# Performance work log

Hardware: AMD Instinct MI355X
Metric: run time of the kernel (lower is better)

The kernel has to match this reference:

```python
import jax, jax.numpy as jnp
import numpy as np

N = 50000
E = 1_600_000
IN_C = 128
HID = 128
HEADS = 4
F_OUT = HID // HEADS  # 32
NEG_SLOPE = 0.2


def _glorot(key, shape):
    fan_in, fan_out = shape[0], shape[-1]
    lim = jnp.sqrt(6.0 / (fan_in + fan_out)).astype(jnp.float32)
    return jax.random.uniform(key, shape, jnp.float32, -lim, lim)


def setup_inputs() -> dict:
    key = jax.random.key(0)
    ks = jax.random.split(key, 12)
    x = jax.random.normal(ks[0], (N, IN_C), jnp.float32)
    edge_index = jax.random.randint(ks[1], (2, E), 0, N, jnp.int32)
    # layer 0 params
    W0 = _glorot(ks[2], (IN_C, HEADS * F_OUT))
    att_src0 = _glorot(ks[3], (HEADS, F_OUT))
    att_dst0 = _glorot(ks[4], (HEADS, F_OUT))
    b0 = jnp.zeros((HEADS * F_OUT,), jnp.float32)
    # layer 1 params
    W1 = _glorot(ks[5], (HID, HEADS * F_OUT))
    att_src1 = _glorot(ks[6], (HEADS, F_OUT))
    att_dst1 = _glorot(ks[7], (HEADS, F_OUT))
    b1 = jnp.zeros((HEADS * F_OUT,), jnp.float32)
    return {"x": x, "edge_index": edge_index,
            "W0": W0, "att_src0": att_src0, "att_dst0": att_dst0, "b0": b0,
            "W1": W1, "att_src1": att_src1, "att_dst1": att_dst1, "b1": b1}


def gat_conv(x, src, dst, W, att_src, att_dst, b):
    n = x.shape[0]
    h = (x @ W).reshape(n, HEADS, F_OUT)              # [N,H,F]
    a_s = jnp.einsum('nhf,hf->nh', h, att_src)        # [N,H]
    a_d = jnp.einsum('nhf,hf->nh', h, att_dst)        # [N,H]
    e = jax.nn.leaky_relu(a_s[src] + a_d[dst], NEG_SLOPE)   # [E,H]
    # segment softmax over destination-node neighborhoods
    e_max = jax.ops.segment_max(e, dst, num_segments=n)     # [N,H]
    e_exp = jnp.exp(e - e_max[dst])                          # [E,H]
    denom = jax.ops.segment_sum(e_exp, dst, num_segments=n)  # [N,H]
    denom = jnp.where(denom > 0, denom, 1.0)
    alpha = e_exp / denom[dst]                               # [E,H]
    msg = alpha[:, :, None] * h[src]                         # [E,H,F]
    out = jax.ops.segment_sum(msg, dst, num_segments=n)      # [N,H,F]
    return out.reshape(n, HEADS * F_OUT) + b


def reference(x, edge_index, W0, att_src0, att_dst0, b0, W1, att_src1, att_dst1, b1):
    src, dst = edge_index[0], edge_index[1]
    h = gat_conv(x, src, dst, W0, att_src0, att_dst0, b0)
    h = jax.nn.relu(h)  # dropout p=0.0 / eval mode -> identity
    out = gat_conv(h, src, dst, W1, att_src1, att_dst1, b1)
    return out
```

## Files before the change

kernel.cpp:

```cpp
#include <hip/hip_runtime.h>
#include <hip/hip_fp16.h>

#define N_NODES 50000
#define N_EDGES 1600000
#define NB 196
#define CAP 8960
#define NBLK_S 512
#define CHUNK_S (N_EDGES / NBLK_S)
#define GEMM_BLOCKS 256

typedef _Float16 half8_t __attribute__((ext_vector_type(8)));
typedef _Float16 half2_t __attribute__((ext_vector_type(2)));
typedef float floatx4 __attribute__((ext_vector_type(4)));

#if defined(__has_builtin)
#  if __has_builtin(__builtin_amdgcn_fdot2)
#    define HAS_FDOT2 1
#  endif
#endif
#ifndef HAS_FDOT2
#  define HAS_FDOT2 0
#endif

__global__ __launch_bounds__(256) void gemm_mfma(const float* __restrict__ Xf,
                                                 const __half* __restrict__ Xh,
                                                 int in_half,
                                                 const float* __restrict__ W,
                                                 const float* __restrict__ att_s,
                                                 const float* __restrict__ att_d,
                                                 __half* __restrict__ H16,
                                                 float* __restrict__ as_out,
                                                 float* __restrict__ ad_out, int nrows,
                                                 const int* __restrict__ e_src,
                                                 const int* __restrict__ e_dst,
                                                 int* __restrict__ bcursor,
                                                 int* __restrict__ bucketed,
                                                 int with_scatter) {
    __shared__ __align__(16) char lds[49152];
    int t = threadIdx.x;
    if (with_scatter && blockIdx.x >= GEMM_BLOCKS) {
        int* recs   = reinterpret_cast<int*>(lds);
        int* srt    = reinterpret_cast<int*>(lds + 12800);
        int* hist   = reinterpret_cast<int*>(lds + 25600);
        int* lstart = reinterpret_cast<int*>(lds + 26624);
        int* curL   = reinterpret_cast<int*>(lds + 27648);
        int* gbase  = reinterpret_cast<int*>(lds + 28672);
        int b = blockIdx.x - GEMM_BLOCKS;
        if (t < NB) hist[t] = 0;
        __syncthreads();
        int s0 = b * CHUNK_S;
        for (int i = t; i < CHUNK_S; i += 256) {
            unsigned sv = (unsigned)e_src[s0 + i], dv = (unsigned)e_dst[s0 + i];
            recs[i] = (int)((sv << 16) | dv);
            atomicAdd(&hist[dv >> 8], 1);
        }
        __syncthreads();
        int myCnt = (t < NB) ? hist[t] : 0;
        if (t < NB) lstart[t] = myCnt;
        __syncthreads();
        for (int o = 1; o < NB; o <<= 1) {
            int v = (t < NB && t >= o) ? lstart[t - o] : 0;
            __syncthreads();
            if (t < NB) lstart[t] += v;
            __syncthreads();
        }
        if (t < NB) {
            int ex = lstart[t] - myCnt;
            lstart[t] = ex;
            curL[t] = ex;
            gbase[t] = t * CAP + atomicAdd(&bcursor[t], myCnt);
        }
        __syncthreads();
        for (int i = t; i < CHUNK_S; i += 256) {
            int r = recs[i];
            int bk = (int)(((unsigned)r & 0xFFFFu) >> 8);
            int p = atomicAdd(&curL[bk], 1);
            srt[p] = r;
        }
        __syncthreads();
        for (int p = t; p < CHUNK_S; p += 256) {
            int r = srt[p];
            unsigned d = (unsigned)r & 0xFFFFu;
            int bk = (int)(d >> 8);
            int g = gbase[bk] + (p - lstart[bk]);
            bucketed[g] = (int)((((unsigned)r >> 16) << 8) | (d & 255u));
        }
        return;
    }
    char* Alds = lds;
    char* Wlds = lds + 16384;
    int lane = t & 63, wv_ = t >> 6;
    for (int p = 0; p < 16; ++p) {
        int flat = p * 256 + t;
        int k = flat >> 5;
        int n0 = (flat & 31) * 4;
        float4 wv = reinterpret_cast<const float4*>(W)[flat];
        const float* wf = reinterpret_cast<const float*>(&wv);
        #pragma unroll
        for (int i = 0; i < 4; ++i) {
            int n = n0 + i;
            int byte = (n * 256 + k * 2) ^ ((n & 7) << 4);
            *reinterpret_cast<__half*>(Wlds + byte) = __float2half(wf[i]);
        }
    }
    int col16 = lane & 15;
    float Asv[8], Adv[8];
    #pragma unroll
    for (int nt = 0; nt < 8; ++nt) {
        Asv[nt] = att_s[nt * 16 + col16];
        Adv[nt] = att_d[nt * 16 + col16];
    }
    int ksub = (lane >> 4) * 16;
    int rloc = wv_ * 16 + col16;
    int ntiles = (nrows + 63) / 64;
    for (int tile = blockIdx.x; tile < ntiles; tile += GEMM_BLOCKS) {
        int row0 = tile * 64;
        __syncthreads();
        for (int p = 0; p < 8; ++p) {
            int r = p * 8 + (t >> 5);
            int f4 = t & 31;
            int rr = row0 + r;
            uint2 hv = make_uint2(0, 0);
            if (rr < nrows) {
                if (in_half) {
                    hv = *reinterpret_cast<const uint2*>(Xh + (size_t)rr * 128 + f4 * 4);
                } else {
                    float4 xv = reinterpret_cast<const float4*>(Xf)[(size_t)rr * 32 + f4];
                    __half2* hp = reinterpret_cast<__half2*>(&hv);
                    hp[0] = __floats2half2_rn(xv.x, xv.y);
                    hp[1] = __floats2half2_rn(xv.z, xv.w);
                }
            }
            int byte = (r * 256 + f4 * 8) ^ ((r & 7) << 4);
            *reinterpret_cast<uint2*>(Alds + byte) = hv;
        }
        __syncthreads();
        half8_t afr[4];
        #pragma unroll
        for (int kb = 0; kb < 4; ++kb) {
            int byte = (rloc * 256 + kb * 64 + ksub) ^ ((rloc & 7) << 4);
            afr[kb] = *reinterpret_cast<half8_t*>(Alds + byte);
        }
        floatx4 acc[8];
        #pragma unroll
        for (int nt = 0; nt < 8; ++nt) {
            int n = nt * 16 + col16;
            floatx4 a = {0.f, 0.f, 0.f, 0.f};
            #pragma unroll
            for (int kb = 0; kb < 4; ++kb) {
                int byte = (n * 256 + kb * 64 + ksub) ^ ((n & 7) << 4);
                half8_t bfr = *reinterpret_cast<half8_t*>(Wlds + byte);
                a = __builtin_amdgcn_mfma_f32_16x16x32_f16(afr[kb], bfr, a, 0, 0, 0);
            }
            acc[nt] = a;
        }
        float ps[4][4], pd[4][4];
        #pragma unroll
        for (int reg = 0; reg < 4; ++reg)
            #pragma unroll
            for (int h = 0; h < 4; ++h) {
                ps[reg][h] = acc[2*h][reg] * Asv[2*h] + acc[2*h+1][reg] * Asv[2*h+1];
                pd[reg][h] = acc[2*h][reg] * Adv[2*h] + acc[2*h+1][reg] * Adv[2*h+1];
            }
        #pragma unroll
        for (int m = 1; m <= 8; m <<= 1)
            #pragma unroll
            for (int reg = 0; reg < 4; ++reg)
                #pragma unroll
                for (int h = 0; h < 4; ++h) {
                    ps[reg][h] += __shfl_xor(ps[reg][h], m);
                    pd[reg][h] += __shfl_xor(pd[reg][h], m);
                }
        int rbase = row0 + wv_ * 16 + (lane >> 4) * 4;
        #pragma unroll
        for (int reg = 0; reg < 4; ++reg) {
            int grow = rbase + reg;
            if (grow < nrows) {
                #pragma unroll
                for (int nt = 0; nt < 8; ++nt)
                    H16[(size_t)grow * 128 + nt * 16 + col16] = __float2half(acc[nt][reg]);
                if (col16 == 0) {
                    *reinterpret_cast<float4*>(as_out + (size_t)grow * 4) =
                        make_float4(ps[reg][0], ps[reg][1], ps[reg][2], ps[reg][3]);
                    *reinterpret_cast<float4*>(ad_out + (size_t)grow * 4) =
                        make_float4(pd[reg][0], pd[reg][1], pd[reg][2], pd[reg][3]);
                }
            }
        }
    }
}

__global__ __launch_bounds__(1024) void bucket_sort(const int* __restrict__ bucketed,
                                                    const int* __restrict__ bcursor,
                                                    int* __restrict__ sorted_packed,
                                                    int* __restrict__ off_s,
                                                    int* __restrict__ off_e) {
    __shared__ int cnt[256], scn[256], cur[256];
    int t = threadIdx.x, k = blockIdx.x;
    int base = k * CAP;
    int m = bcursor[k];
    if (t < 256) cnt[t] = 0;
    __syncthreads();
    for (int i = t; i < m; i += 1024)
        atomicAdd(&cnt[bucketed[base + i] & 255], 1);
    __syncthreads();
    if (t < 256) scn[t] = cnt[t];
    __syncthreads();
    for (int o = 1; o < 256; o <<= 1) {
        int v = (t < 256 && t >= o) ? scn[t - o] : 0;
        __syncthreads();
        if (t < 256) scn[t] += v;
        __syncthreads();
    }
    if (t < 256) {
        int excl = scn[t] - cnt[t];
        cur[t] = base + excl;
        int node = k * 256 + t;
        if (node < N_NODES) {
            off_s[node] = base + excl;
            off_e[node] = base + excl + cnt[t];
        }
    }
    __syncthreads();
    for (int i = t; i < m; i += 1024) {
        int rec = bucketed[base + i];
        int p = atomicAdd(&cur[rec & 255], 1);
        sorted_packed[p] = rec;
    }
}

__global__ __launch_bounds__(256) void gat_aggregate_v3(const __half* __restrict__ H16,
                                                        const int* __restrict__ off_s,
                                                        const int* __restrict__ off_e,
                                                        const int* __restrict__ packed,
                                                        const float* __restrict__ asb,
                                                        const float* __restrict__ adb,
                                                        const float* __restrict__ bias,
                                                        float* __restrict__ OUTF,
                                                        __half* __restrict__ OUTH,
                                                        int n, int mode) {
    int wid = (blockIdx.x * 256 + threadIdx.x) >> 6;
    int lane = threadIdx.x & 63;
    if (wid >= n) return;
    int s = off_s[wid], e = off_e[wid];
    int q = lane >> 4;
    int sub = lane & 15;
    int head4 = (sub >> 2) * 4;
    int sub16 = sub * 16;
    float adv = adb[(size_t)wid * 4 + (sub >> 2)];
    const char* Hc = reinterpret_cast<const char*>(H16);
    const char* Ac = reinterpret_cast<const char*>(asb);
    float acc[8] = {0, 0, 0, 0, 0, 0, 0, 0};
    float den = 0.f;
    if (s < e) {
        int idx[4]; float sc[4];
        #pragma unroll
        for (int u = 0; u < 4; ++u) {
            int ii = s + q + u * 4;
            int jj = ii < e ? ii : s;
            idx[u] = packed[jj] & 0xFFFFFF00;
            sc[u] = *reinterpret_cast<const float*>(Ac + (idx[u] >> 4) + head4);
        }
        for (int i = s; i < e; i += 16) {
            uint4 h0 = *reinterpret_cast<const uint4*>(Hc + idx[0] + sub16);
            uint4 h1 = *reinterpret_cast<const uint4*>(Hc + idx[1] + sub16);
            uint4 h2 = *reinterpret_cast<const uint4*>(Hc + idx[2] + sub16);
            uint4 h3 = *reinterpret_cast<const uint4*>(Hc + idx[3] + sub16);
            float w[4];
            #pragma unroll
            for (int u = 0; u < 4; ++u) {
                float ev = sc[u] + adv; ev = fmaxf(ev, 0.2f * ev);
                w[u] = (i + q + u * 4 < e) ? __expf(ev) : 0.f;
            }
            #pragma unroll
            for (int u = 0; u < 4; ++u) {
                int ii = i + 16 + q + u * 4;
                int jj = ii < e ? ii : s;
                idx[u] = packed[jj] & 0xFFFFFF00;
                sc[u] = *reinterpret_cast<const float*>(Ac + (idx[u] >> 4) + head4);
            }
            den += (w[0] + w[1]) + (w[2] + w[3]);
#if HAS_FDOT2
            half2_t w01 = __builtin_bit_cast(half2_t, __builtin_amdgcn_cvt_pkrtz(w[0], w[1]));
            half2_t w23 = __builtin_bit_cast(half2_t, __builtin_amdgcn_cvt_pkrtz(w[2], w[3]));
            const uint* a0 = reinterpret_cast<const uint*>(&h0);
            const uint* a1 = reinterpret_cast<const uint*>(&h1);
            const uint* a2 = reinterpret_cast<const uint*>(&h2);
            const uint* a3 = reinterpret_cast<const uint*>(&h3);
            #pragma unroll
            for (int j = 0; j < 4; ++j) {
                uint p0 = __builtin_amdgcn_perm(a1[j], a0[j], 0x05040100u);
                uint p1 = __builtin_amdgcn_perm(a1[j], a0[j], 0x07060302u);
                uint r0 = __builtin_amdgcn_perm(a3[j], a2[j], 0x05040100u);
                uint r1 = __builtin_amdgcn_perm(a3[j], a2[j], 0x07060302u);
                acc[2*j]   = __builtin_amdgcn_fdot2(__builtin_bit_cast(half2_t, p0), w01,
                             __builtin_amdgcn_fdot2(__builtin_bit_cast(half2_t, r0), w23, acc[2*j],   false), false);
                acc[2*j+1] = __builtin_amdgcn_fdot2(__builtin_bit_cast(half2_t, p1), w01,
                             __builtin_amdgcn_fdot2(__builtin_bit_cast(half2_t, r1), w23, acc[2*j+1], false), false);
            }
#else
            const __half2* pa = reinterpret_cast<const __half2*>(&h0);
            const __half2* pb = reinterpret_cast<const __half2*>(&h1);
            const __half2* pc = reinterpret_cast<const __half2*>(&h2);
            const __half2* pd_ = reinterpret_cast<const __half2*>(&h3);
            #pragma unroll
            for (int j = 0; j < 4; ++j) {
                float2 fa = __half22float2(pa[j]);
                float2 fb = __half22float2(pb[j]);
                float2 fc = __half22float2(pc[j]);
                float2 fd = __half22float2(pd_[j]);
                acc[2*j]   += w[0] * fa.x + w[1] * fb.x + w[2] * fc.x + w[3] * fd.x;
                acc[2*j+1] += w[0] * fa.y + w[1] * fb.y + w[2] * fc.y + w[3] * fd.y;
            }
#endif
        }
    }
    #pragma unroll
    for (int j = 0; j < 8; ++j) acc[j] += __shfl_xor(acc[j], 16);
    den += __shfl_xor(den, 16);
    #pragma unroll
    for (int j = 0; j < 8; ++j) acc[j] += __shfl_xor(acc[j], 32);
    den += __shfl_xor(den, 32);
    if (q == 0) {
        float inv = den > 0.f ? 1.f / den : 0.f;
        float4 b0 = *reinterpret_cast<const float4*>(bias + sub * 8);
        float4 b1 = *reinterpret_cast<const float4*>(bias + sub * 8 + 4);
        float o[8];
        o[0] = acc[0]*inv + b0.x; o[1] = acc[1]*inv + b0.y;
        o[2] = acc[2]*inv + b0.z; o[3] = acc[3]*inv + b0.w;
        o[4] = acc[4]*inv + b1.x; o[5] = acc[5]*inv + b1.y;
        o[6] = acc[6]*inv + b1.z; o[7] = acc[7]*inv + b1.w;
        if (mode) {
            uint4 u;
            __half2* up = reinterpret_cast<__half2*>(&u);
            #pragma unroll
            for (int j = 0; j < 4; ++j)
                up[j] = __floats2half2_rn(fmaxf(o[2*j], 0.f), fmaxf(o[2*j+1], 0.f));
            *reinterpret_cast<uint4*>(OUTH + (size_t)wid * 128 + sub * 8) = u;
        } else {
            *reinterpret_cast<float4*>(OUTF + (size_t)wid * 128 + sub * 8) =
                make_float4(o[0], o[1], o[2], o[3]);
            *reinterpret_cast<float4*>(OUTF + (size_t)wid * 128 + sub * 8 + 4) =
                make_float4(o[4], o[5], o[6], o[7]);
        }
    }
}

extern "C" void kernel_launch(void* const* d_in, const int* in_sizes, int n_in,
                              void* d_out, int out_size, void* d_ws, size_t ws_size,
                              hipStream_t stream) {
    const float* x        = (const float*)d_in[0];
    const int*   edge     = (const int*)d_in[1];
    const float* W0       = (const float*)d_in[2];
    const float* att_src0 = (const float*)d_in[3];
    const float* att_dst0 = (const float*)d_in[4];
    const float* b0       = (const float*)d_in[5];
    const float* W1       = (const float*)d_in[6];
    const float* att_src1 = (const float*)d_in[7];
    const float* att_dst1 = (const float*)d_in[8];
    const float* b1       = (const float*)d_in[9];
    const int* src = edge;
    const int* dst = edge + N_EDGES;
    float* out = (float*)d_out;

    char* ws = (char*)d_ws;
    size_t o = 0;
    auto alloc = [&](size_t bytes) { char* p = ws + o; o += (bytes + 255) & ~(size_t)255; return p; };
    __half* H16   = (__half*)alloc((size_t)N_NODES * 128 * 2);
    float* asb    = (float*)alloc((size_t)N_NODES * 4 * 4);
    float* adb    = (float*)alloc((size_t)N_NODES * 4 * 4);
    int*   off_s  = (int*)alloc((size_t)N_NODES * 4);
    int*   off_e  = (int*)alloc((size_t)N_NODES * 4);
    int*   sorted = (int*)alloc((size_t)NB * CAP * 4);
    size_t mark = o;
    int*   bcursor  = (int*)alloc((size_t)NB * 4);
    int*   bucketed = (int*)alloc((size_t)NB * CAP * 4);
    o = mark + (size_t)N_NODES * 128 * 2;
    __half* h1_16 = (__half*)(ws + mark);

    hipMemsetAsync(bcursor, 0, (size_t)NB * 4, stream);
    gemm_mfma<<<GEMM_BLOCKS + NBLK_S, 256, 0, stream>>>(x, (const __half*)nullptr, 0,
                                                        W0, att_src0, att_dst0,
                                                        H16, asb, adb, N_NODES,
                                                        src, dst, bcursor, bucketed, 1);
    bucket_sort<<<NB, 1024, 0, stream>>>(bucketed, bcursor, sorted, off_s, off_e);

    int agg_blocks = N_NODES / 4;

    gat_aggregate_v3<<<agg_blocks, 256, 0, stream>>>(H16, off_s, off_e, sorted, asb, adb, b0,
                                                     (float*)nullptr, h1_16, N_NODES, 1);

    gemm_mfma<<<GEMM_BLOCKS, 256, 0, stream>>>((const float*)nullptr, h1_16, 1,
                                               W1, att_src1, att_dst1,
                                               H16, asb, adb, N_NODES,
                                               (const int*)nullptr, (const int*)nullptr,
                                               (int*)nullptr, (int*)nullptr, 0);
    gat_aggregate_v3<<<agg_blocks, 256, 0, stream>>>(H16, off_s, off_e, sorted, asb, adb, b1,
                                                     out, (__half*)nullptr, N_NODES, 0);
}
```

Baseline: 189.7 us.

## Precompute swizzled fp16 weight images, cache bucket records in LDS, widen layer-1 GEMM grid

```diff
diff --git a/kernel.cpp b/kernel.cpp
--- a/kernel.cpp
+++ b/kernel.cpp
@@ -7,7 +7,8 @@
 #define CAP 8960
 #define NBLK_S 512
 #define CHUNK_S (N_EDGES / NBLK_S)
-#define GEMM_BLOCKS 256
+#define GEMM0_BLOCKS 256
+#define GEMM1_BLOCKS 768
 
 typedef _Float16 half8_t __attribute__((ext_vector_type(8)));
 typedef _Float16 half2_t __attribute__((ext_vector_type(2)));
@@ -22,15 +23,35 @@
 #  define HAS_FDOT2 0
 #endif
 
+__global__ __launch_bounds__(256) void prep(const float* __restrict__ W0,
+                                            const float* __restrict__ W1,
+                                            __half* __restrict__ img0,
+                                            __half* __restrict__ img1,
+                                            int* __restrict__ bcursor) {
+    int t = threadIdx.x, b = blockIdx.x;
+    const float* W = b ? W1 : W0;
+    char* img = reinterpret_cast<char*>(b ? img1 : img0);
+    int n = t & 127;
+    int k0 = (t >> 7) * 64;
+    for (int kk = 0; kk < 64; ++kk) {
+        int k = k0 + kk;
+        float v = W[(size_t)k * 128 + n];
+        int byte = (n * 256 + k * 2) ^ ((n & 7) << 4);
+        *reinterpret_cast<__half*>(img + byte) = __float2half(v);
+    }
+    if (b == 0 && t < NB) bcursor[t] = 0;
+}
+
 __global__ __launch_bounds__(256) void gemm_mfma(const float* __restrict__ Xf,
                                                  const __half* __restrict__ Xh,
                                                  int in_half,
-                                                 const float* __restrict__ W,
+                                                 const __half* __restrict__ Wimg,
                                                  const float* __restrict__ att_s,
                                                  const float* __restrict__ att_d,
                                                  __half* __restrict__ H16,
                                                  float* __restrict__ as_out,
                                                  float* __restrict__ ad_out, int nrows,
+                                                 int ngemm,
                                                  const int* __restrict__ e_src,
                                                  const int* __restrict__ e_dst,
                                                  int* __restrict__ bcursor,
@@ -38,14 +59,14 @@
                                                  int with_scatter) {
     __shared__ __align__(16) char lds[49152];
     int t = threadIdx.x;
-    if (with_scatter && blockIdx.x >= GEMM_BLOCKS) {
+    if (with_scatter && blockIdx.x >= ngemm) {
         int* recs   = reinterpret_cast<int*>(lds);
         int* srt    = reinterpret_cast<int*>(lds + 12800);
         int* hist   = reinterpret_cast<int*>(lds + 25600);
         int* lstart = reinterpret_cast<int*>(lds + 26624);
         int* curL   = reinterpret_cast<int*>(lds + 27648);
         int* gbase  = reinterpret_cast<int*>(lds + 28672);
-        int b = blockIdx.x - GEMM_BLOCKS;
+        int b = blockIdx.x - ngemm;
         if (t < NB) hist[t] = 0;
         __syncthreads();
         int s0 = b * CHUNK_S;
@@ -90,18 +111,11 @@
     char* Alds = lds;
     char* Wlds = lds + 16384;
     int lane = t & 63, wv_ = t >> 6;
-    for (int p = 0; p < 16; ++p) {
-        int flat = p * 256 + t;
-        int k = flat >> 5;
-        int n0 = (flat & 31) * 4;
-        float4 wv = reinterpret_cast<const float4*>(W)[flat];
-        const float* wf = reinterpret_cast<const float*>(&wv);
-        #pragma unroll
-        for (int i = 0; i < 4; ++i) {
-            int n = n0 + i;
-            int byte = (n * 256 + k * 2) ^ ((n & 7) << 4);
-            *reinterpret_cast<__half*>(Wlds + byte) = __float2half(wf[i]);
-        }
+    {
+        const uint4* wi = reinterpret_cast<const uint4*>(Wimg);
+        uint4* wl = reinterpret_cast<uint4*>(Wlds);
+        #pragma unroll
+        for (int p = 0; p < 8; ++p) wl[p * 256 + t] = wi[p * 256 + t];
     }
     int col16 = lane & 15;
     float Asv[8], Adv[8];
@@ -113,7 +127,7 @@
     int ksub = (lane >> 4) * 16;
     int rloc = wv_ * 16 + col16;
     int ntiles = (nrows + 63) / 64;
-    for (int tile = blockIdx.x; tile < ntiles; tile += GEMM_BLOCKS) {
+    for (int tile = blockIdx.x; tile < ntiles; tile += ngemm) {
         int row0 = tile * 64;
         __syncthreads();
         for (int p = 0; p < 8; ++p) {
@@ -195,14 +209,18 @@
                                                     int* __restrict__ sorted_packed,
                                                     int* __restrict__ off_s,
                                                     int* __restrict__ off_e) {
+    __shared__ int recs[CAP];
     __shared__ int cnt[256], scn[256], cur[256];
     int t = threadIdx.x, k = blockIdx.x;
     int base = k * CAP;
     int m = bcursor[k];
     if (t < 256) cnt[t] = 0;
     __syncthreads();
-    for (int i = t; i < m; i += 1024)
-        atomicAdd(&cnt[bucketed[base + i] & 255], 1);
+    for (int i = t; i < m; i += 1024) {
+        int r = bucketed[base + i];
+        recs[i] = r;
+        atomicAdd(&cnt[r & 255], 1);
+    }
     __syncthreads();
     if (t < 256) scn[t] = cnt[t];
     __syncthreads();
@@ -223,7 +241,7 @@
     }
     __syncthreads();
     for (int i = t; i < m; i += 1024) {
-        int rec = bucketed[base + i];
+        int rec = recs[i];
         int p = atomicAdd(&cur[rec & 255], 1);
         sorted_packed[p] = rec;
     }
@@ -372,17 +390,20 @@
     int*   off_s  = (int*)alloc((size_t)N_NODES * 4);
     int*   off_e  = (int*)alloc((size_t)N_NODES * 4);
     int*   sorted = (int*)alloc((size_t)NB * CAP * 4);
+    __half* img0  = (__half*)alloc(32768);
+    __half* img1  = (__half*)alloc(32768);
     size_t mark = o;
     int*   bcursor  = (int*)alloc((size_t)NB * 4);
     int*   bucketed = (int*)alloc((size_t)NB * CAP * 4);
     o = mark + (size_t)N_NODES * 128 * 2;
     __half* h1_16 = (__half*)(ws + mark);
 
-    hipMemsetAsync(bcursor, 0, (size_t)NB * 4, stream);
-    gemm_mfma<<<GEMM_BLOCKS + NBLK_S, 256, 0, stream>>>(x, (const __half*)nullptr, 0,
-                                                        W0, att_src0, att_dst0,
-                                                        H16, asb, adb, N_NODES,
-                                                        src, dst, bcursor, bucketed, 1);
+    prep<<<2, 256, 0, stream>>>(W0, W1, img0, img1, bcursor);
+
+    gemm_mfma<<<GEMM0_BLOCKS + NBLK_S, 256, 0, stream>>>(x, (const __half*)nullptr, 0,
+                                                         img0, att_src0, att_dst0,
+                                                         H16, asb, adb, N_NODES, GEMM0_BLOCKS,
+                                                         src, dst, bcursor, bucketed, 1);
     bucket_sort<<<NB, 1024, 0, stream>>>(bucketed, bcursor, sorted, off_s, off_e);
 
     int agg_blocks = N_NODES / 4;
@@ -390,11 +411,11 @@
     gat_aggregate_v3<<<agg_blocks, 256, 0, stream>>>(H16, off_s, off_e, sorted, asb, adb, b0,
                                                      (float*)nullptr, h1_16, N_NODES, 1);
 
-    gemm_mfma<<<GEMM_BLOCKS, 256, 0, stream>>>((const float*)nullptr, h1_16, 1,
-                                               W1, att_src1, att_dst1,
-                                               H16, asb, adb, N_NODES,
-                                               (const int*)nullptr, (const int*)nullptr,
-                                               (int*)nullptr, (int*)nullptr, 0);
+    gemm_mfma<<<GEMM1_BLOCKS, 256, 0, stream>>>((const float*)nullptr, h1_16, 1,
+                                                img1, att_src1, att_dst1,
+                                                H16, asb, adb, N_NODES, GEMM1_BLOCKS,
+                                                (const int*)nullptr, (const int*)nullptr,
+                                                (int*)nullptr, (int*)nullptr, 0);
     gat_aggregate_v3<<<agg_blocks, 256, 0, stream>>>(H16, off_s, off_e, sorted, asb, adb, b1,
                                                      out, (__half*)nullptr, N_NODES, 0);
 }
```

After: 184.4 us. -2.8%, faster.
